# Kernel optimization log

Measured on AMD Instinct MI355X. Metric: run time of the kernel, lower is better.

## Reference

```python
import jax, jax.numpy as jnp
import numpy as np

D_MODEL = 1024
D_HIDDEN = 4096
NUM_EXPERTS = 8
B, T = 2, 2048


def setup_inputs() -> dict:
    key = jax.random.key(0)
    ks = jax.random.split(key, 8)
    s = 0.02
    x = jax.random.normal(ks[0], (B, T, D_MODEL), dtype=jnp.float32)
    Wg = jax.random.normal(ks[1], (D_MODEL, NUM_EXPERTS), dtype=jnp.float32) * s
    bg = jnp.zeros((NUM_EXPERTS,), dtype=jnp.float32)
    W1 = jax.random.normal(ks[2], (NUM_EXPERTS, D_MODEL, D_HIDDEN), dtype=jnp.float32) * s
    b1 = jnp.zeros((NUM_EXPERTS, D_HIDDEN), dtype=jnp.float32)
    W2 = jax.random.normal(ks[3], (NUM_EXPERTS, D_HIDDEN, D_MODEL), dtype=jnp.float32) * s
    b2 = jnp.zeros((NUM_EXPERTS, D_MODEL), dtype=jnp.float32)
    return {"x": x, "Wg": Wg, "bg": bg, "W1": W1, "b1": b1, "W2": W2, "b2": b2}


def reference(x, Wg, bg, W1, b1, W2, b2):
    # Gating: top-1 routing
    gate_logits = jnp.einsum('btd,de->bte', x, Wg) + bg          # (B,T,E)
    gate_scores = jax.nn.softmax(gate_logits, axis=-1)
    top1_idx = jnp.argmax(gate_scores, axis=-1)                   # (B,T)
    top1_mask = jax.nn.one_hot(top1_idx, NUM_EXPERTS, dtype=x.dtype)  # (B,T,E)
    top1_weight = jnp.sum(gate_scores * top1_mask, axis=-1, keepdims=True)  # (B,T,1)

    # Dense all-expert compute (faithful to the naive original), then mask.
    # For unselected tokens the original computes expert(0)*0 = 0, identical
    # to expert(x)*0 = 0 here.
    h = jax.nn.silu(jnp.einsum('btd,edh->bteh', x, W1) + b1)      # (B,T,E,H)
    o = jnp.einsum('bteh,ehd->bted', h, W2) + b2                  # (B,T,E,D)
    y = jnp.sum(o * top1_mask[..., None], axis=2) * top1_weight   # (B,T,D)
    return y
```

## Files before the change

kernel.cpp:

```cpp
#include <hip/hip_runtime.h>
#include <stdint.h>

#define D_MODEL 1024
#define D_HIDDEN 4096
#define NUM_EXPERTS 8
#define NTOK 4096
#define MAXSLOT1 24
#define MAXSLOT2 40

typedef __bf16 bf16x8 __attribute__((ext_vector_type(8)));
typedef float floatx4 __attribute__((ext_vector_type(4)));
typedef unsigned int uint2e __attribute__((ext_vector_type(2)));
typedef unsigned int uint4e __attribute__((ext_vector_type(4)));

static __device__ __forceinline__ unsigned short f2bf(float f) {
    union { float f; unsigned int i; } v;
    v.f = f;
    unsigned int i = v.i;
    unsigned int r = (i + 0x7fffu + ((i >> 16) & 1u)) >> 16;
    return (unsigned short)r;
}

static __device__ __forceinline__ void gl_lds16(const unsigned short* g, unsigned short* l) {
    __builtin_amdgcn_global_load_lds(
        (const __attribute__((address_space(1))) void*)g,
        (__attribute__((address_space(3))) void*)l, 16, 0, 0);
}

#define TRRD(dst, addr, off)                                   \
    asm volatile("ds_read_b64_tr_b16 %0, %1 offset:" #off      \
                 : "=v"(dst) : "v"(addr) : "memory")

static __device__ __forceinline__ bf16x8 pack_tr(uint2e a, uint2e b) {
    uint4e p; p.x = a.x; p.y = a.y; p.z = b.x; p.w = b.y;
    return __builtin_bit_cast(bf16x8, p);
}

__global__ __launch_bounds__(256) void convgate_kernel(
    const float* __restrict__ x,
    const float* __restrict__ Wg,
    const float* __restrict__ bg,
    const float* __restrict__ W1,
    const float* __restrict__ W2,
    int* __restrict__ counts,
    int* __restrict__ tlist,
    float* __restrict__ wgt,
    unsigned short* __restrict__ xb,
    unsigned short* __restrict__ w1c,
    unsigned short* __restrict__ w2c)
{
    const int tid = threadIdx.x;
    if (blockIdx.x < 8192) {
        const int half = blockIdx.x >> 12;
        const float* src = half ? W2 : W1;
        unsigned short* dst = half ? w2c : w1c;
        const size_t c0 = ((size_t)(blockIdx.x & 4095) * 256 + tid) * 8;
        float4 v[8];
#pragma unroll
        for (int q = 0; q < 4; ++q) {
            const float* s = src + c0 + (size_t)q * 8388608;
            v[q * 2]     = *(const float4*)(s);
            v[q * 2 + 1] = *(const float4*)(s + 4);
        }
#pragma unroll
        for (int q = 0; q < 4; ++q) {
            uint4 o;
            o.x = (unsigned)f2bf(v[q*2].x)   | ((unsigned)f2bf(v[q*2].y) << 16);
            o.y = (unsigned)f2bf(v[q*2].z)   | ((unsigned)f2bf(v[q*2].w) << 16);
            o.z = (unsigned)f2bf(v[q*2+1].x) | ((unsigned)f2bf(v[q*2+1].y) << 16);
            o.w = (unsigned)f2bf(v[q*2+1].z) | ((unsigned)f2bf(v[q*2+1].w) << 16);
            *(uint4*)(dst + c0 + (size_t)q * 8388608) = o;
        }
        return;
    }

    const int wave = tid >> 6;
    const int lane = tid & 63;
    const int tok = (blockIdx.x - 8192) * 4 + wave;

    float acc[NUM_EXPERTS];
#pragma unroll
    for (int e = 0; e < NUM_EXPERTS; e++) acc[e] = 0.f;

    const float4* xr = (const float4*)(x + (size_t)tok * D_MODEL);
    unsigned int* xbr = (unsigned int*)(xb + (size_t)tok * D_MODEL);

#pragma unroll
    for (int i = 0; i < 4; i++) {
        int d4 = i * 64 + lane;
        float4 v = xr[d4];
        unsigned int p0 = (unsigned int)f2bf(v.x) | ((unsigned int)f2bf(v.y) << 16);
        unsigned int p1 = (unsigned int)f2bf(v.z) | ((unsigned int)f2bf(v.w) << 16);
        uint2 pk; pk.x = p0; pk.y = p1;
        *(uint2*)&xbr[d4 * 2] = pk;

        float vc[4] = {v.x, v.y, v.z, v.w};
#pragma unroll
        for (int c = 0; c < 4; c++) {
            const float4* wr = (const float4*)(Wg + (size_t)(d4 * 4 + c) * NUM_EXPERTS);
            float4 w0 = wr[0], w1 = wr[1];
            acc[0] += vc[c] * w0.x; acc[1] += vc[c] * w0.y;
            acc[2] += vc[c] * w0.z; acc[3] += vc[c] * w0.w;
            acc[4] += vc[c] * w1.x; acc[5] += vc[c] * w1.y;
            acc[6] += vc[c] * w1.z; acc[7] += vc[c] * w1.w;
        }
    }
#pragma unroll
    for (int e = 0; e < NUM_EXPERTS; e++) {
        float v = acc[e];
#pragma unroll
        for (int off = 32; off > 0; off >>= 1) v += __shfl_xor(v, off, 64);
        acc[e] = v;
    }
    if (lane == 0) {
        float lg[NUM_EXPERTS];
#pragma unroll
        for (int e = 0; e < NUM_EXPERTS; e++) lg[e] = acc[e] + bg[e];
        int amax = 0;
        float m = lg[0];
#pragma unroll
        for (int e = 1; e < NUM_EXPERTS; e++) {
            if (lg[e] > m) { m = lg[e]; amax = e; }
        }
        float s = 0.f;
#pragma unroll
        for (int e = 0; e < NUM_EXPERTS; e++) s += __expf(lg[e] - m);
        wgt[tok] = 1.0f / s;
        int pos = atomicAdd(&counts[amax], 1);
        tlist[amax * NTOK + pos] = tok;
    }
}

__device__ __forceinline__ bool slot_to_expert(const int* counts, int slot, int shift,
                                               int& e_out, int& mt_out, int& cnt_out) {
    int cum = 0;
    for (int i = 0; i < NUM_EXPERTS; i++) {
        int c = counts[i];
        int tt = (c + (1 << shift) - 1) >> shift;
        if (slot < cum + tt) {
            e_out = i; mt_out = slot - cum; cnt_out = c;
            return true;
        }
        cum += tt;
    }
    return false;
}

__global__ __launch_bounds__(512, 2) void ffn1_kernel(
    const unsigned short* __restrict__ xb,
    const unsigned short* __restrict__ w1c,
    const float* __restrict__ b1,
    const int* __restrict__ counts,
    const int* __restrict__ tlist,
    unsigned short* __restrict__ h)
{
    int e, mt, cnt;
    if (!slot_to_expert(counts, blockIdx.y, 8, e, mt, cnt)) return;
    const int n0 = blockIdx.x * 256;

    __shared__ __align__(16) unsigned short Al[2][256 * 64];
    __shared__ __align__(16) unsigned short Bl[2][256 * 64];
    __shared__ int toks[256];

    const int tid = threadIdx.x;
    if (tid < 256) {
        int r = mt * 256 + tid;
        toks[tid] = (r < cnt) ? tlist[e * NTOK + r] : -1;
    }
    __syncthreads();

    const int wave = tid >> 6, lane = tid & 63;
    const int quad = lane >> 4, lm = lane & 15;
    const int mo = (wave >> 2) * 128, wc = wave & 3;
    const int no = wc * 64;

    const unsigned short* w1e = w1c + (size_t)e * D_MODEL * D_HIDDEN;
    const int ag = ((tid & 7) ^ ((tid >> 3) & 7)) * 8;
    const unsigned short* asrc[4];
#pragma unroll
    for (int j = 0; j < 4; ++j) {
        int m = j * 64 + (tid >> 3);
        int tk = toks[m];
        asrc[j] = xb + (size_t)(tk < 0 ? 0 : tk) * D_MODEL + ag;
    }
    const int bk = (tid >> 1) & 63, bn8 = (tid & 1) * 8;
    const unsigned short* bsrc[4];
#pragma unroll
    for (int j = 0; j < 4; ++j) {
        int nb = j * 4 + (tid >> 7);
        bsrc[j] = w1e + (size_t)bk * D_HIDDEN + n0 + nb * 16 + bn8;
    }

#define F1_STAGE(p, k0)                                                  \
    do {                                                                 \
        _Pragma("unroll")                                                \
        for (int j = 0; j < 4; ++j)                                      \
            gl_lds16(asrc[j] + (k0), &Al[p][j * 4096 + wave * 512]);     \
        _Pragma("unroll")                                                \
        for (int j = 0; j < 4; ++j)                                      \
            gl_lds16(bsrc[j] + (size_t)(k0) * D_HIDDEN,                  \
                     &Bl[p][j * 4096 + wave * 512]);                     \
    } while (0)

#define F1_COMPUTE(p)                                                         \
    do {                                                                      \
        const unsigned short* Ab = &Al[p][0];                                 \
        const unsigned bvB = (unsigned)(uintptr_t)&Bl[p][0]                   \
                           + (unsigned)(wc * 8192 + quad * 256 + lm * 8);     \
        _Pragma("unroll")                                                     \
        for (int s = 0; s < 2; ++s) {                                         \
            bf16x8 af[8];                                                     \
            const int gsw = ((s * 4 + quad) ^ (lm & 7)) * 8;                  \
            _Pragma("unroll")                                                 \
            for (int i = 0; i < 8; ++i)                                       \
                af[i] = *(const bf16x8*)(Ab + (mo + i * 16 + lm) * 64 + gsw); \
            uint2e t0, t1, t2, t3, t4, t5, t6, t7;                            \
            const unsigned vs = bvB + s * 1024;                               \
            unsigned v0 = vs, v1 = vs + 2048, v2 = vs + 4096, v3 = vs + 6144; \
            TRRD(t0, v0, 0); TRRD(t1, v0, 128);                               \
            TRRD(t2, v1, 0); TRRD(t3, v1, 128);                               \
            TRRD(t4, v2, 0); TRRD(t5, v2, 128);                               \
            TRRD(t6, v3, 0); TRRD(t7, v3, 128);                               \
            asm volatile("s_waitcnt lgkmcnt(0)" ::: "memory");                \
            __builtin_amdgcn_sched_barrier(0);                                \
            bf16x8 bf[4];                                                     \
            bf[0] = pack_tr(t0, t1); bf[1] = pack_tr(t2, t3);                 \
            bf[2] = pack_tr(t4, t5); bf[3] = pack_tr(t6, t7);                 \
            _Pragma("unroll")                                                 \
            for (int i = 0; i < 8; ++i)                                       \
                _Pragma("unroll")                                             \
                for (int j = 0; j < 4; ++j)                                   \
                    acc[i][j] = __builtin_amdgcn_mfma_f32_16x16x32_bf16(      \
                        af[i], bf[j], acc[i][j], 0, 0, 0);                    \
        }                                                                     \
    } while (0)

    floatx4 acc[8][4];
#pragma unroll
    for (int i = 0; i < 8; i++)
#pragma unroll
        for (int j = 0; j < 4; j++) acc[i][j] = (floatx4){0.f, 0.f, 0.f, 0.f};

    const int NT = D_MODEL / 64;
    F1_STAGE(0, 0);
    __syncthreads();
    int cur = 0;
    for (int kt = 1; kt < NT; ++kt) {
        F1_STAGE(cur ^ 1, kt * 64);
        F1_COMPUTE(cur);
        __syncthreads();
        cur ^= 1;
    }
    F1_COMPUTE(cur);

    const float* b1e = b1 + (size_t)e * D_HIDDEN;
#pragma unroll
    for (int ni = 0; ni < 4; ++ni) {
        int n = n0 + no + ni * 16 + lm;
        float bias = b1e[n];
#pragma unroll
        for (int mi = 0; mi < 8; ++mi)
#pragma unroll
            for (int r = 0; r < 4; ++r) {
                int m = mo + mi * 16 + quad * 4 + r;
                int tk = toks[m];
                if (tk >= 0) {
                    float z = acc[mi][ni][r] + bias;
                    h[(size_t)tk * D_HIDDEN + n] = f2bf(z / (1.f + __expf(-z)));
                }
            }
    }
}

__global__ __launch_bounds__(256, 2) void ffn2_kernel(
    const unsigned short* __restrict__ h,
    const unsigned short* __restrict__ w2c,
    const float* __restrict__ b2,
    const int* __restrict__ counts,
    const int* __restrict__ tlist,
    const float* __restrict__ wgt,
    float* __restrict__ out)
{
    int e, mt, cnt;
    if (!slot_to_expert(counts, blockIdx.y, 7, e, mt, cnt)) return;
    const int n0 = blockIdx.x * 128;

    __shared__ __align__(16) unsigned short Al[2][128 * 64];
    __shared__ __align__(16) unsigned short Bl[2][128 * 64];
    __shared__ int toks[128];

    const int tid = threadIdx.x;
    if (tid < 128) {
        int r = mt * 128 + tid;
        toks[tid] = (r < cnt) ? tlist[e * NTOK + r] : -1;
    }
    __syncthreads();

    const int wave = tid >> 6, lane = tid & 63;
    const int quad = lane >> 4, lm = lane & 15;
    const int mo = (wave & 1) * 64, wc = wave >> 1;
    const int no = wc * 64;

    const unsigned short* w2e = w2c + (size_t)e * D_MODEL * D_HIDDEN;
    const int ag = ((tid & 7) ^ ((tid >> 3) & 7)) * 8;
    const unsigned short* asrc[4];
#pragma unroll
    for (int j = 0; j < 4; ++j) {
        int m = j * 32 + (tid >> 3);
        int tk = toks[m];
        asrc[j] = h + (size_t)(tk < 0 ? 0 : tk) * D_HIDDEN + ag;
    }
    const int bk = (tid >> 1) & 63, bn8 = (tid & 1) * 8;
    const unsigned short* bsrc[4];
#pragma unroll
    for (int j = 0; j < 4; ++j) {
        int nb = j * 2 + (tid >> 7);
        bsrc[j] = w2e + (size_t)bk * D_MODEL + n0 + nb * 16 + bn8;
    }

#define F2_STAGE(p, k0)                                                  \
    do {                                                                 \
        _Pragma("unroll")                                                \
        for (int j = 0; j < 4; ++j)                                      \
            gl_lds16(asrc[j] + (k0), &Al[p][j * 2048 + wave * 512]);     \
        _Pragma("unroll")                                                \
        for (int j = 0; j < 4; ++j)                                      \
            gl_lds16(bsrc[j] + (size_t)(k0) * D_MODEL,                   \
                     &Bl[p][j * 2048 + wave * 512]);                     \
    } while (0)

#define F2_COMPUTE(p)                                                         \
    do {                                                                      \
        const unsigned short* Ab = &Al[p][0];                                 \
        const unsigned bvB = (unsigned)(uintptr_t)&Bl[p][0]                   \
                           + (unsigned)(wc * 8192 + quad * 256 + lm * 8);     \
        _Pragma("unroll")                                                     \
        for (int s = 0; s < 2; ++s) {                                         \
            bf16x8 af[4];                                                     \
            const int gsw = ((s * 4 + quad) ^ (lm & 7)) * 8;                  \
            _Pragma("unroll")                                                 \
            for (int i = 0; i < 4; ++i)                                       \
                af[i] = *(const bf16x8*)(Ab + (mo + i * 16 + lm) * 64 + gsw); \
            uint2e t0, t1, t2, t3, t4, t5, t6, t7;                            \
            const unsigned vs = bvB + s * 1024;                               \
            unsigned v0 = vs, v1 = vs + 2048, v2 = vs + 4096, v3 = vs + 6144; \
            TRRD(t0, v0, 0); TRRD(t1, v0, 128);                               \
            TRRD(t2, v1, 0); TRRD(t3, v1, 128);                               \
            TRRD(t4, v2, 0); TRRD(t5, v2, 128);                               \
            TRRD(t6, v3, 0); TRRD(t7, v3, 128);                               \
            asm volatile("s_waitcnt lgkmcnt(0)" ::: "memory");                \
            __builtin_amdgcn_sched_barrier(0);                                \
            bf16x8 bf[4];                                                     \
            bf[0] = pack_tr(t0, t1); bf[1] = pack_tr(t2, t3);                 \
            bf[2] = pack_tr(t4, t5); bf[3] = pack_tr(t6, t7);                 \
            _Pragma("unroll")                                                 \
            for (int i = 0; i < 4; ++i)                                       \
                _Pragma("unroll")                                             \
                for (int j = 0; j < 4; ++j)                                   \
                    acc[i][j] = __builtin_amdgcn_mfma_f32_16x16x32_bf16(      \
                        af[i], bf[j], acc[i][j], 0, 0, 0);                    \
        }                                                                     \
    } while (0)

    floatx4 acc[4][4];
#pragma unroll
    for (int i = 0; i < 4; i++)
#pragma unroll
        for (int j = 0; j < 4; j++) acc[i][j] = (floatx4){0.f, 0.f, 0.f, 0.f};

    const int NT = D_HIDDEN / 64;
    F2_STAGE(0, 0);
    __syncthreads();
    int cur = 0;
    for (int kt = 1; kt < NT; ++kt) {
        F2_STAGE(cur ^ 1, kt * 64);
        F2_COMPUTE(cur);
        __syncthreads();
        cur ^= 1;
    }
    F2_COMPUTE(cur);

    const float* b2e = b2 + (size_t)e * D_MODEL;
#pragma unroll
    for (int ni = 0; ni < 4; ++ni) {
        int n = n0 + no + ni * 16 + lm;
        float bias = b2e[n];
#pragma unroll
        for (int mi = 0; mi < 4; ++mi)
#pragma unroll
            for (int r = 0; r < 4; ++r) {
                int m = mo + mi * 16 + quad * 4 + r;
                int tk = toks[m];
                if (tk >= 0) {
                    out[(size_t)tk * D_MODEL + n] = (acc[mi][ni][r] + bias) * wgt[tk];
                }
            }
    }
}

extern "C" void kernel_launch(void* const* d_in, const int* in_sizes, int n_in,
                              void* d_out, int out_size, void* d_ws, size_t ws_size,
                              hipStream_t stream) {
    const float* x  = (const float*)d_in[0];
    const float* Wg = (const float*)d_in[1];
    const float* bg = (const float*)d_in[2];
    const float* W1 = (const float*)d_in[3];
    const float* b1 = (const float*)d_in[4];
    const float* W2 = (const float*)d_in[5];
    const float* b2 = (const float*)d_in[6];
    float* out = (float*)d_out;

    char* ws = (char*)d_ws;
    int*   counts = (int*)ws;
    float* wgt    = (float*)(ws + 1024);
    int*   tlist  = (int*)(ws + 32768);
    unsigned short* xb   = (unsigned short*)(ws + 262144);
    unsigned short* hbuf = (unsigned short*)(ws + 8650752);
    unsigned short* w1c  = (unsigned short*)(ws + 42205184);
    unsigned short* w2c  = (unsigned short*)(ws + 109314048);

    hipMemsetAsync(counts, 0, NUM_EXPERTS * sizeof(int), stream);

    convgate_kernel<<<9216, 256, 0, stream>>>(x, Wg, bg, W1, W2,
                                              counts, tlist, wgt, xb, w1c, w2c);
    ffn1_kernel<<<dim3(D_HIDDEN / 256, MAXSLOT1), 512, 0, stream>>>(
        xb, w1c, b1, counts, tlist, hbuf);
    ffn2_kernel<<<dim3(D_MODEL / 128, MAXSLOT2), 256, 0, stream>>>(
        hbuf, w2c, b2, counts, tlist, wgt, out);
}
```

Baseline: 563.8 us.

## Deepen ffn2 prefetch pipeline with vmcnt waits and use nontemporal weight loads

The ffn2 main loop now issues two stages of global-to-LDS loads ahead and waits with s_waitcnt vmcnt(8) plus raw s_barrier, replacing the full __syncthreads per iteration, so loads for tile k+1 stay in flight while tile k is computed. The weight conversion in convgate uses nontemporal loads to avoid polluting cache, and the gating blocks are moved to the front of the grid so routing finishes earlier. The hand-written vmcnt count depends on the exact number of loads per stage, so a mismatch would cause a race.

```diff
diff --git a/kernel.cpp b/kernel.cpp
--- a/kernel.cpp
+++ b/kernel.cpp
@@ -10,6 +10,7 @@
 
 typedef __bf16 bf16x8 __attribute__((ext_vector_type(8)));
 typedef float floatx4 __attribute__((ext_vector_type(4)));
+typedef float f32x4v __attribute__((ext_vector_type(4)));
 typedef unsigned int uint2e __attribute__((ext_vector_type(2)));
 typedef unsigned int uint4e __attribute__((ext_vector_type(4)));
 
@@ -50,17 +51,18 @@
     unsigned short* __restrict__ w2c)
 {
     const int tid = threadIdx.x;
-    if (blockIdx.x < 8192) {
-        const int half = blockIdx.x >> 12;
+    if (blockIdx.x >= 1024) {
+        const int bid = blockIdx.x - 1024;
+        const int half = bid >> 12;
         const float* src = half ? W2 : W1;
         unsigned short* dst = half ? w2c : w1c;
-        const size_t c0 = ((size_t)(blockIdx.x & 4095) * 256 + tid) * 8;
-        float4 v[8];
+        const size_t c0 = ((size_t)(bid & 4095) * 256 + tid) * 8;
+        f32x4v v[8];
 #pragma unroll
         for (int q = 0; q < 4; ++q) {
-            const float* s = src + c0 + (size_t)q * 8388608;
-            v[q * 2]     = *(const float4*)(s);
-            v[q * 2 + 1] = *(const float4*)(s + 4);
+            const f32x4v* s = (const f32x4v*)(src + c0 + (size_t)q * 8388608);
+            v[q * 2]     = __builtin_nontemporal_load(s);
+            v[q * 2 + 1] = __builtin_nontemporal_load(s + 1);
         }
 #pragma unroll
         for (int q = 0; q < 4; ++q) {
@@ -76,7 +78,7 @@
 
     const int wave = tid >> 6;
     const int lane = tid & 63;
-    const int tok = (blockIdx.x - 8192) * 4 + wave;
+    const int tok = blockIdx.x * 4 + wave;
 
     float acc[NUM_EXPERTS];
 #pragma unroll
@@ -370,15 +372,22 @@
 
     const int NT = D_HIDDEN / 64;
     F2_STAGE(0, 0);
-    __syncthreads();
-    int cur = 0;
-    for (int kt = 1; kt < NT; ++kt) {
-        F2_STAGE(cur ^ 1, kt * 64);
-        F2_COMPUTE(cur);
-        __syncthreads();
-        cur ^= 1;
-    }
-    F2_COMPUTE(cur);
+    F2_STAGE(1, 64);
+
+    for (int kt = 0; kt < NT; ++kt) {
+        const int p = kt & 1;
+        if (kt + 1 < NT) asm volatile("s_waitcnt vmcnt(8)" ::: "memory");
+        else             asm volatile("s_waitcnt vmcnt(0)" ::: "memory");
+        __builtin_amdgcn_s_barrier();
+        __builtin_amdgcn_sched_barrier(0);
+        F2_COMPUTE(p);
+        if (kt + 1 < NT) {
+            __builtin_amdgcn_sched_barrier(0);
+            __builtin_amdgcn_s_barrier();
+            __builtin_amdgcn_sched_barrier(0);
+            if (kt + 2 < NT) F2_STAGE(p, (kt + 2) * 64);
+        }
+    }
 
     const float* b2e = b2 + (size_t)e * D_MODEL;
 #pragma unroll
@@ -419,7 +428,7 @@
     unsigned short* w1c  = (unsigned short*)(ws + 42205184);
     unsigned short* w2c  = (unsigned short*)(ws + 109314048);
 
-    hipMemsetAsync(counts, 0, NUM_EXPERTS * sizeof(int), stream);
+    (void)hipMemsetAsync(counts, 0, NUM_EXPERTS * sizeof(int), stream);
 
     convgate_kernel<<<9216, 256, 0, stream>>>(x, Wg, bg, W1, W2,
                                               counts, tlist, wgt, xb, w1c, w2c);
```

Result: faster. 524.8 us (-6.9%).
